# Kernel optimization log

Hardware: AMD Instinct MI355X
Metric: run time of the kernel (lower is better)

The kernel has to match this reference:

```python
import math
import jax, jax.numpy as jnp
import numpy as np

B, S, D = 64, 729, 64  # S = (32*14//16 - 1)**2

def setup_inputs() -> dict:
    key = jax.random.key(0)
    kq, kk, kv, km = jax.random.split(key, 4)
    return {
        "query": jax.random.normal(kq, (B, S, D), dtype=jnp.float32),
        "key": jax.random.normal(kk, (B, S, D), dtype=jnp.float32),
        "value": jax.random.normal(kv, (B, S, D), dtype=jnp.float32),
        "mask": jax.random.randint(km, (B, S, S), 0, 2, dtype=jnp.int32),
    }

def reference(query, key, value, mask):
    dk = query.shape[-1]
    # [B,S,S] scores
    scores = jnp.einsum('bqd,bkd->bqk', query, key) / math.sqrt(dk)
    scores = jnp.where(mask == 0, jnp.float32(-1e9), scores)
    attention = jnp.tanh(scores)  # args.activation == 'tanh'
    # ignore_diag == 1: zero the diagonal of each [S,S] attention map
    eye = jnp.eye(attention.shape[-1], dtype=attention.dtype)
    attention = attention * (1.0 - eye)
    out = jnp.einsum('bqk,bkd->bqd', attention, value)
    return (out, attention)
```

## Files before the change

### kernel.cpp

```cpp
#include <hip/hip_runtime.h>

#define BATCH 64
#define SEQ 729
#define DIM 64
#define NT 12
#define STRB 72
#define MSTR 68
#define OSTR 68

typedef __attribute__((ext_vector_type(8))) short bf16x8;
typedef __attribute__((ext_vector_type(4))) float f32x4;
typedef int   i32x4a __attribute__((ext_vector_type(4), aligned(4)));
typedef float f32x4a __attribute__((ext_vector_type(4), aligned(4)));

__device__ __forceinline__ unsigned short f2bf(float f) {
    unsigned int u = __float_as_uint(f);
    u += 0x7fffu + ((u >> 16) & 1u);
    return (unsigned short)(u >> 16);
}

__device__ __forceinline__ unsigned long long pack4bf(float a, float b, float c, float d) {
    return (unsigned long long)f2bf(a)
         | ((unsigned long long)f2bf(b) << 16)
         | ((unsigned long long)f2bf(c) << 32)
         | ((unsigned long long)f2bf(d) << 48);
}

__device__ __forceinline__ float bf2f(unsigned int hi16) {
    return __uint_as_float(hi16 << 16);
}

__device__ __forceinline__ float fast_tanh(float x) {
    float e = __builtin_amdgcn_exp2f(x * 2.88539008177792681f);
    return 1.0f - 2.0f * __builtin_amdgcn_rcpf(e + 1.0f);
}

#define BAR() do { \
    asm volatile("s_waitcnt lgkmcnt(0)" ::: "memory"); \
    __builtin_amdgcn_s_barrier(); \
    __builtin_amdgcn_sched_barrier(0); \
} while (0)

__global__ __launch_bounds__(256, 3) void attn_kernel(
    const float* __restrict__ Qg, const float* __restrict__ Kg,
    const float* __restrict__ Vg, const int* __restrict__ Mg,
    float* __restrict__ Og, float* __restrict__ Ag)
{
    __shared__ __align__(16) unsigned char smem[50432];
    unsigned short* Ks0 = (unsigned short*)(smem);
    unsigned short* Vs0 = (unsigned short*)(smem + 9216);
    unsigned short* Ks1 = (unsigned short*)(smem + 18432);
    unsigned short* Vs1 = (unsigned short*)(smem + 27648);
    unsigned short* Ps  = (unsigned short*)(smem + 36864);
    unsigned char*  Mb8 = smem + 46080;
    float* Ostage = (float*)smem;

    const int tid = threadIdx.x;
    const int q0  = blockIdx.x * 64;
    const int b   = blockIdx.y;

    const float* Qb = Qg + (size_t)b * SEQ * DIM;
    const float* Kb = Kg + (size_t)b * SEQ * DIM;
    const float* Vb = Vg + (size_t)b * SEQ * DIM;
    const int*   Mb = Mg + (size_t)b * SEQ * SEQ;
    float* Ob = Og + (size_t)b * SEQ * DIM;
    float* Ab = Ag + (size_t)b * SEQ * SEQ;

    const int lane = tid & 63;
    const int quad = lane >> 4;
    const int l15  = lane & 15;
    const int qrow = (tid >> 6) * 16;

    const int rr = tid >> 4;
    const int cc = (tid & 15) * 4;
    const int vd0 = (tid & 15) * 4;
    const int vk0 = (tid >> 4) * 4;
    const int prow = qrow + (lane >> 4);
    const int pcol = (lane & 15) * 4;

    float4 kr[4], vr[4];
    i32x4a mr[4];

    auto load_k = [&](int k0n) {
        #pragma unroll
        for (int i = 0; i < 4; ++i) {
            int gk = k0n + rr + 16 * i;
            kr[i] = (gk < SEQ) ? *(const float4*)(Kb + gk * DIM + cc)
                               : float4{0, 0, 0, 0};
        }
    };
    auto load_v = [&](int k0n) {
        #pragma unroll
        for (int i = 0; i < 4; ++i) {
            int gk = k0n + vk0 + i;
            vr[i] = (gk < SEQ) ? *(const float4*)(Vb + gk * DIM + vd0)
                               : float4{0, 0, 0, 0};
        }
    };
    auto load_mask = [&](int k0n) {
        #pragma unroll
        for (int i = 0; i < 4; ++i) {
            int gq = q0 + prow + 4 * i;
            int gk = k0n + pcol;
            if (gq < SEQ && gk + 3 < SEQ) {
                mr[i] = *(const i32x4a*)(Mb + (size_t)gq * SEQ + gk);
            } else if (gq < SEQ) {
                i32x4a t;
                #pragma unroll
                for (int e = 0; e < 4; ++e)
                    t[e] = (gk + e < SEQ) ? Mb[(size_t)gq * SEQ + gk + e] : 0;
                mr[i] = t;
            } else {
                mr[i] = i32x4a{0, 0, 0, 0};
            }
        }
    };
    auto drain_mask = [&]() {
        #pragma unroll
        for (int i = 0; i < 4; ++i) {
            unsigned int mb = (unsigned)(mr[i][0] & 1)
                            | ((unsigned)(mr[i][1] & 1) << 8)
                            | ((unsigned)(mr[i][2] & 1) << 16)
                            | ((unsigned)(mr[i][3] & 1) << 24);
            *(unsigned int*)&Mb8[(prow + 4 * i) * MSTR + pcol] = mb;
        }
    };
    auto drain_kv = [&](unsigned short* Kd, unsigned short* Vd) {
        #pragma unroll
        for (int i = 0; i < 4; ++i)
            *(unsigned long long*)&Kd[(rr + 16 * i) * STRB + cc] =
                pack4bf(kr[i].x, kr[i].y, kr[i].z, kr[i].w);
        #pragma unroll
        for (int j = 0; j < 4; ++j) {
            float v0 = j==0?vr[0].x:j==1?vr[0].y:j==2?vr[0].z:vr[0].w;
            float v1 = j==0?vr[1].x:j==1?vr[1].y:j==2?vr[1].z:vr[1].w;
            float v2 = j==0?vr[2].x:j==1?vr[2].y:j==2?vr[2].z:vr[2].w;
            float v3 = j==0?vr[3].x:j==1?vr[3].y:j==2?vr[3].z:vr[3].w;
            *(unsigned long long*)&Vd[(vd0 + j) * STRB + vk0] = pack4bf(v0, v1, v2, v3);
        }
    };

    load_k(0); load_v(0); load_mask(0);
    #pragma unroll
    for (int i = 0; i < 4; ++i) {
        int gq = q0 + rr + 16 * i;
        float4 x = (gq < SEQ) ? *(const float4*)(Qb + gq * DIM + cc)
                              : float4{0, 0, 0, 0};
        *(unsigned long long*)&Ps[(rr + 16 * i) * STRB + cc] = pack4bf(x.x, x.y, x.z, x.w);
    }
    BAR();

    const bf16x8 aq0 = *(const bf16x8*)&Ps[(qrow + l15) * STRB + quad * 8];
    const bf16x8 aq1 = *(const bf16x8*)&Ps[(qrow + l15) * STRB + 32 + quad * 8];

    drain_mask();
    drain_kv(Ks0, Vs0);
    load_k(64); load_v(64); load_mask(64);
    BAR();

    f32x4 oacc[4];
    #pragma unroll
    for (int dt = 0; dt < 4; ++dt) {
        oacc[dt][0]=0.f; oacc[dt][1]=0.f; oacc[dt][2]=0.f; oacc[dt][3]=0.f;
    }

    for (int t = 0; t < NT; ++t) {
        const int k0 = t * 64;
        const unsigned short* KsC = (t & 1) ? Ks1 : Ks0;
        const unsigned short* VsC = (t & 1) ? Vs1 : Vs0;
        unsigned short* KsN = (t & 1) ? Ks0 : Ks1;
        unsigned short* VsN = (t & 1) ? Vs0 : Vs1;

        f32x4 sacc[4];
        #pragma unroll
        for (int n = 0; n < 4; ++n) {
            bf16x8 bk0 = *(const bf16x8*)&KsC[(n * 16 + l15) * STRB + quad * 8];
            bf16x8 bk1 = *(const bf16x8*)&KsC[(n * 16 + l15) * STRB + 32 + quad * 8];
            f32x4 c; c[0]=0.f; c[1]=0.f; c[2]=0.f; c[3]=0.f;
            c = __builtin_amdgcn_mfma_f32_16x16x32_bf16(aq0, bk0, c, 0, 0, 0);
            c = __builtin_amdgcn_mfma_f32_16x16x32_bf16(aq1, bk1, c, 0, 0, 0);
            sacc[n] = c;
        }

        #pragma unroll
        for (int n = 0; n < 4; ++n) {
            int col = n * 16 + l15;
            int gk  = k0 + col;
            #pragma unroll
            for (int r = 0; r < 4; ++r) {
                int qloc = qrow + quad * 4 + r;
                int gq = q0 + qloc;
                int m = Mb8[qloc * MSTR + col];
                float sv = sacc[n][r] * 0.125f;
                float p = fast_tanh((m == 0) ? -1e9f : sv);
                if (gq == gk || gk >= SEQ) p = 0.0f;
                Ps[qloc * STRB + col] = f2bf(p);
            }
        }

        const bf16x8 ap0 = *(const bf16x8*)&Ps[(qrow + l15) * STRB + quad * 8];
        const bf16x8 ap1 = *(const bf16x8*)&Ps[(qrow + l15) * STRB + 32 + quad * 8];
        #pragma unroll
        for (int dt = 0; dt < 4; ++dt) {
            bf16x8 bv0 = *(const bf16x8*)&VsC[(dt * 16 + l15) * STRB + quad * 8];
            bf16x8 bv1 = *(const bf16x8*)&VsC[(dt * 16 + l15) * STRB + 32 + quad * 8];
            oacc[dt] = __builtin_amdgcn_mfma_f32_16x16x32_bf16(ap0, bv0, oacc[dt], 0, 0, 0);
            oacc[dt] = __builtin_amdgcn_mfma_f32_16x16x32_bf16(ap1, bv1, oacc[dt], 0, 0, 0);
        }

        #pragma unroll
        for (int i = 0; i < 4; ++i) {
            int row = prow + 4 * i;
            int gq  = q0 + row;
            int gk  = k0 + pcol;
            unsigned long long w = *(const unsigned long long*)&Ps[row * STRB + pcol];
            f32x4 pv;
            pv[0] = bf2f((unsigned)(w      ) & 0xffffu);
            pv[1] = bf2f((unsigned)(w >> 16) & 0xffffu);
            pv[2] = bf2f((unsigned)(w >> 32) & 0xffffu);
            pv[3] = bf2f((unsigned)(w >> 48) & 0xffffu);
            if (gq < SEQ) {
                if (gk + 3 < SEQ) {
                    *(f32x4a*)(Ab + (size_t)gq * SEQ + gk) = pv;
                } else {
                    #pragma unroll
                    for (int e = 0; e < 4; ++e)
                        if (gk + e < SEQ) Ab[(size_t)gq * SEQ + gk + e] = pv[e];
                }
            }
        }

        if (t + 1 < NT) {
            drain_mask();
            drain_kv(KsN, VsN);
            if (t + 2 < NT) {
                load_k(k0 + 128); load_v(k0 + 128); load_mask(k0 + 128);
            }
            BAR();
        }
    }

    BAR();
    #pragma unroll
    for (int dt = 0; dt < 4; ++dt)
        #pragma unroll
        for (int r = 0; r < 4; ++r)
            Ostage[(qrow + quad * 4 + r) * OSTR + dt * 16 + l15] = oacc[dt][r];
    #pragma unroll
    for (int i = 0; i < 4; ++i) {
        int row = prow + 4 * i;
        int gq  = q0 + row;
        f32x4 ov = *(const f32x4*)&Ostage[row * OSTR + pcol];
        if (gq < SEQ) *(f32x4*)(Ob + (size_t)gq * DIM + pcol) = ov;
    }
}

extern "C" void kernel_launch(void* const* d_in, const int* in_sizes, int n_in,
                              void* d_out, int out_size, void* d_ws, size_t ws_size,
                              hipStream_t stream) {
    const float* Q = (const float*)d_in[0];
    const float* K = (const float*)d_in[1];
    const float* V = (const float*)d_in[2];
    const int*   M = (const int*)d_in[3];
    float* Out  = (float*)d_out;
    float* Attn = Out + (size_t)BATCH * SEQ * DIM;
    dim3 grid(NT, BATCH);
    attn_kernel<<<grid, 256, 0, stream>>>(Q, K, V, M, Out, Attn);
}
```

Baseline: 324.9 us.

## Switch to 32x32x16 MFMA with 2x2 wave tiling of the score tile

```diff
diff --git a/kernel.cpp b/kernel.cpp
--- a/kernel.cpp
+++ b/kernel.cpp
@@ -10,6 +10,7 @@
 
 typedef __attribute__((ext_vector_type(8))) short bf16x8;
 typedef __attribute__((ext_vector_type(4))) float f32x4;
+typedef __attribute__((ext_vector_type(16))) float f32x16;
 typedef int   i32x4a __attribute__((ext_vector_type(4), aligned(4)));
 typedef float f32x4a __attribute__((ext_vector_type(4), aligned(4)));
 
@@ -41,7 +42,9 @@
     __builtin_amdgcn_sched_barrier(0); \
 } while (0)
 
-__global__ __launch_bounds__(256, 3) void attn_kernel(
+__global__ __launch_bounds__(256)
+__attribute__((amdgpu_waves_per_eu(3, 3)))
+void attn_kernel(
     const float* __restrict__ Qg, const float* __restrict__ Kg,
     const float* __restrict__ Vg, const int* __restrict__ Mg,
     float* __restrict__ Og, float* __restrict__ Ag)
@@ -67,15 +70,17 @@
     float* Ab = Ag + (size_t)b * SEQ * SEQ;
 
     const int lane = tid & 63;
-    const int quad = lane >> 4;
-    const int l15  = lane & 15;
-    const int qrow = (tid >> 6) * 16;
+    const int l31  = lane & 31;
+    const int lh   = lane >> 5;
+    const int wid  = tid >> 6;
+    const int wr   = wid >> 1;
+    const int wc   = wid & 1;
 
     const int rr = tid >> 4;
     const int cc = (tid & 15) * 4;
     const int vd0 = (tid & 15) * 4;
     const int vk0 = (tid >> 4) * 4;
-    const int prow = qrow + (lane >> 4);
+    const int prow = (wid * 16) + (lane >> 4);
     const int pcol = (lane & 15) * 4;
 
     float4 kr[4], vr[4];
@@ -150,19 +155,19 @@
     }
     BAR();
 
-    const bf16x8 aq0 = *(const bf16x8*)&Ps[(qrow + l15) * STRB + quad * 8];
-    const bf16x8 aq1 = *(const bf16x8*)&Ps[(qrow + l15) * STRB + 32 + quad * 8];
+    bf16x8 aq[4];
+    #pragma unroll
+    for (int t = 0; t < 4; ++t)
+        aq[t] = *(const bf16x8*)&Ps[(32 * wr + l31) * STRB + 16 * t + 8 * lh];
 
     drain_mask();
     drain_kv(Ks0, Vs0);
     load_k(64); load_v(64); load_mask(64);
     BAR();
 
-    f32x4 oacc[4];
-    #pragma unroll
-    for (int dt = 0; dt < 4; ++dt) {
-        oacc[dt][0]=0.f; oacc[dt][1]=0.f; oacc[dt][2]=0.f; oacc[dt][3]=0.f;
-    }
+    f32x16 oacc;
+    #pragma unroll
+    for (int r = 0; r < 16; ++r) oacc[r] = 0.0f;
 
     for (int t = 0; t < NT; ++t) {
         const int k0 = t * 64;
@@ -171,63 +176,59 @@
         unsigned short* KsN = (t & 1) ? Ks0 : Ks1;
         unsigned short* VsN = (t & 1) ? Vs0 : Vs1;
 
-        f32x4 sacc[4];
-        #pragma unroll
-        for (int n = 0; n < 4; ++n) {
-            bf16x8 bk0 = *(const bf16x8*)&KsC[(n * 16 + l15) * STRB + quad * 8];
-            bf16x8 bk1 = *(const bf16x8*)&KsC[(n * 16 + l15) * STRB + 32 + quad * 8];
-            f32x4 c; c[0]=0.f; c[1]=0.f; c[2]=0.f; c[3]=0.f;
-            c = __builtin_amdgcn_mfma_f32_16x16x32_bf16(aq0, bk0, c, 0, 0, 0);
-            c = __builtin_amdgcn_mfma_f32_16x16x32_bf16(aq1, bk1, c, 0, 0, 0);
-            sacc[n] = c;
-        }
-
-        #pragma unroll
-        for (int n = 0; n < 4; ++n) {
-            int col = n * 16 + l15;
-            int gk  = k0 + col;
-            #pragma unroll
-            for (int r = 0; r < 4; ++r) {
-                int qloc = qrow + quad * 4 + r;
-                int gq = q0 + qloc;
-                int m = Mb8[qloc * MSTR + col];
-                float sv = sacc[n][r] * 0.125f;
-                float p = fast_tanh((m == 0) ? -1e9f : sv);
-                if (gq == gk || gk >= SEQ) p = 0.0f;
-                Ps[qloc * STRB + col] = f2bf(p);
-            }
-        }
-
-        const bf16x8 ap0 = *(const bf16x8*)&Ps[(qrow + l15) * STRB + quad * 8];
-        const bf16x8 ap1 = *(const bf16x8*)&Ps[(qrow + l15) * STRB + 32 + quad * 8];
-        #pragma unroll
-        for (int dt = 0; dt < 4; ++dt) {
-            bf16x8 bv0 = *(const bf16x8*)&VsC[(dt * 16 + l15) * STRB + quad * 8];
-            bf16x8 bv1 = *(const bf16x8*)&VsC[(dt * 16 + l15) * STRB + 32 + quad * 8];
-            oacc[dt] = __builtin_amdgcn_mfma_f32_16x16x32_bf16(ap0, bv0, oacc[dt], 0, 0, 0);
-            oacc[dt] = __builtin_amdgcn_mfma_f32_16x16x32_bf16(ap1, bv1, oacc[dt], 0, 0, 0);
-        }
-
-        #pragma unroll
-        for (int i = 0; i < 4; ++i) {
-            int row = prow + 4 * i;
-            int gq  = q0 + row;
-            int gk  = k0 + pcol;
-            unsigned long long w = *(const unsigned long long*)&Ps[row * STRB + pcol];
-            f32x4 pv;
-            pv[0] = bf2f((unsigned)(w      ) & 0xffffu);
-            pv[1] = bf2f((unsigned)(w >> 16) & 0xffffu);
-            pv[2] = bf2f((unsigned)(w >> 32) & 0xffffu);
-            pv[3] = bf2f((unsigned)(w >> 48) & 0xffffu);
+        f32x16 sacc;
+        #pragma unroll
+        for (int r = 0; r < 16; ++r) sacc[r] = 0.0f;
+        #pragma unroll
+        for (int tt = 0; tt < 4; ++tt) {
+            bf16x8 bk = *(const bf16x8*)&KsC[(32 * wc + l31) * STRB + 16 * tt + 8 * lh];
+            sacc = __builtin_amdgcn_mfma_f32_32x32x16_bf16(aq[tt], bk, sacc, 0, 0, 0);
+        }
+
+        #pragma unroll
+        for (int r = 0; r < 16; ++r) {
+            int qloc = 32 * wr + (r & 3) + 8 * (r >> 2) + 4 * lh;
+            int kloc = 32 * wc + l31;
+            int gq = q0 + qloc;
+            int gk = k0 + kloc;
+            int m = Mb8[qloc * MSTR + kloc];
+            float sv = sacc[r] * 0.125f;
+            float p = fast_tanh((m == 0) ? -1e9f : sv);
+            if (gq == gk || gk >= SEQ) p = 0.0f;
+            Ps[qloc * STRB + kloc] = f2bf(p);
+        }
+
+        #pragma unroll
+        for (int i = 0; i < 2; ++i) {
+            int rloc = 32 * wr + (lane >> 2) + 16 * i;
+            int gq   = q0 + rloc;
+            int gk   = k0 + 32 * wc + 8 * (lane & 3);
+            bf16x8 w = *(const bf16x8*)&Ps[rloc * STRB + 32 * wc + 8 * (lane & 3)];
             if (gq < SEQ) {
-                if (gk + 3 < SEQ) {
-                    *(f32x4a*)(Ab + (size_t)gq * SEQ + gk) = pv;
+                if (gk + 7 < SEQ) {
+                    f32x4a v0, v1;
+                    v0[0] = bf2f((unsigned short)w[0]); v0[1] = bf2f((unsigned short)w[1]);
+                    v0[2] = bf2f((unsigned short)w[2]); v0[3] = bf2f((unsigned short)w[3]);
+                    v1[0] = bf2f((unsigned short)w[4]); v1[1] = bf2f((unsigned short)w[5]);
+                    v1[2] = bf2f((unsigned short)w[6]); v1[3] = bf2f((unsigned short)w[7]);
+                    *(f32x4a*)(Ab + (size_t)gq * SEQ + gk)     = v0;
+                    *(f32x4a*)(Ab + (size_t)gq * SEQ + gk + 4) = v1;
                 } else {
                     #pragma unroll
-                    for (int e = 0; e < 4; ++e)
-                        if (gk + e < SEQ) Ab[(size_t)gq * SEQ + gk + e] = pv[e];
+                    for (int e = 0; e < 8; ++e)
+                        if (gk + e < SEQ)
+                            Ab[(size_t)gq * SEQ + gk + e] = bf2f((unsigned short)w[e]);
                 }
             }
+        }
+
+        BAR();
+
+        #pragma unroll
+        for (int tt = 0; tt < 4; ++tt) {
+            bf16x8 ap = *(const bf16x8*)&Ps[(32 * wr + l31) * STRB + 16 * tt + 8 * lh];
+            bf16x8 bv = *(const bf16x8*)&VsC[(32 * wc + l31) * STRB + 16 * tt + 8 * lh];
+            oacc = __builtin_amdgcn_mfma_f32_32x32x16_bf16(ap, bv, oacc, 0, 0, 0);
         }
 
         if (t + 1 < NT) {
@@ -240,15 +241,15 @@
         }
     }
 
+    #pragma unroll
+    for (int r = 0; r < 16; ++r) {
+        int row = 32 * wr + (r & 3) + 8 * (r >> 2) + 4 * lh;
+        Ostage[row * OSTR + 32 * wc + l31] = oacc[r];
+    }
     BAR();
     #pragma unroll
-    for (int dt = 0; dt < 4; ++dt)
-        #pragma unroll
-        for (int r = 0; r < 4; ++r)
-            Ostage[(qrow + quad * 4 + r) * OSTR + dt * 16 + l15] = oacc[dt][r];
-    #pragma unroll
     for (int i = 0; i < 4; ++i) {
-        int row = prow + 4 * i;
+        int row = 16 * wid + (lane >> 4) + 4 * i;
         int gq  = q0 + row;
         f32x4 ov = *(const f32x4*)&Ostage[row * OSTR + pcol];
         if (gq < SEQ) *(f32x4*)(Ob + (size_t)gq * DIM + pcol) = ov;
```

New measurement: 330.7 us. No clear change (+1.8%).
